# Kernel optimization log

Measured on AMD Instinct MI355X. Metric: run time of the kernel, lower is better.

## Reference

```python
import jax, jax.numpy as jnp
import numpy as np

K = 3
PAD = 1
KP = K * K


def setup_inputs() -> dict:
    key = jax.random.key(0)
    k1, k2, k3, k4 = jax.random.split(key, 4)
    B, C, O, H, W = 8, 64, 64, 128, 128
    x = jax.random.normal(k1, (B, C, H, W), dtype=jnp.float32)
    offset = jax.random.normal(k2, (B, 2 * KP, H, W), dtype=jnp.float32)
    weight = jax.random.normal(k3, (O, C, K, K), dtype=jnp.float32) * 0.05
    bias = jax.random.normal(k4, (O,), dtype=jnp.float32) * 0.05
    return {"x": x, "offset": offset, "weight": weight, "bias": bias}


def _deform_conv(x, offset, weight, bias):
    B, C, H, W = x.shape
    O = weight.shape[0]
    x_pad = jnp.pad(x, ((0, 0), (0, 0), (PAD, PAD), (PAD, PAD)))
    Hp, Wp = H + 2 * PAD, W + 2 * PAD
    dt = x.dtype

    # kernel-point grid, row-major (yy, xx) as in torch meshgrid 'ij'
    r = K // 2
    rng = jnp.arange(-r, r + 1, dtype=dt)
    ky = jnp.repeat(rng, K)          # [KP]
    kx = jnp.tile(rng, K)            # [KP]

    base_y = jnp.arange(H, dtype=dt) + PAD
    base_x = jnp.arange(W, dtype=dt) + PAD

    off = offset.reshape(B, KP, 2, H, W)
    # sample coords in padded-image space; grid_sample align_corners=True
    # normalization cancels exactly, so sample at (cy, cx) directly.
    cy = base_y[None, None, :, None] + ky[None, :, None, None] + off[:, :, 0]  # [B,KP,H,W]
    cx = base_x[None, None, None, :] + kx[None, :, None, None] + off[:, :, 1]

    y0 = jnp.floor(cy)
    x0 = jnp.floor(cx)
    wy1 = cy - y0
    wx1 = cx - x0
    wy0 = 1.0 - wy1
    wx0 = 1.0 - wx1

    flat = x_pad.reshape(B, C, Hp * Wp)

    def gather(yi, xi):
        # zeros padding: out-of-bounds corner pixels contribute 0
        valid = ((yi >= 0) & (yi <= Hp - 1) & (xi >= 0) & (xi <= Wp - 1)).astype(dt)
        yc = jnp.clip(yi, 0, Hp - 1).astype(jnp.int32)
        xc = jnp.clip(xi, 0, Wp - 1).astype(jnp.int32)
        idx = (yc * Wp + xc).reshape(B, 1, KP * H * W)
        g = jnp.take_along_axis(flat, jnp.broadcast_to(idx, (B, C, KP * H * W)), axis=2)
        g = g.reshape(B, C, KP, H, W)
        return g * valid[:, None]  # broadcast valid [B,1,KP,H,W]

    sampled = (wy0 * wx0)[:, None] * gather(y0, x0) \
            + (wy0 * wx1)[:, None] * gather(y0, x0 + 1) \
            + (wy1 * wx0)[:, None] * gather(y0 + 1, x0) \
            + (wy1 * wx1)[:, None] * gather(y0 + 1, x0 + 1)  # [B,C,KP,H,W]

    w3 = weight.reshape(O, C, KP)
    out = jnp.einsum('bcphw,ocp->bohw', sampled, w3) + bias[None, :, None, None]
    return out


def reference(x, offset, weight, bias):
    return _deform_conv(x, offset, weight, bias)
```

## Files before the change

kernel.cpp:

```cpp
#include <hip/hip_runtime.h>
#include <hip/hip_bf16.h>

#define BB 8
#define CC 64
#define OO 64
#define HH 128
#define WW 128
#define HP 130
#define WP 130
#define KP 9

typedef __attribute__((ext_vector_type(8))) short bf16x8;
typedef __attribute__((ext_vector_type(4))) float f32x4;
typedef __attribute__((ext_vector_type(4))) unsigned u32x4;

static __device__ __forceinline__ unsigned short f2bf(float f) {
  unsigned u = __float_as_uint(f);
  unsigned r = u + 0x7fffu + ((u >> 16) & 1u);
  return (unsigned short)(r >> 16);
}
static __device__ __forceinline__ f32x4 unpk4(unsigned lo, unsigned hi) {
  f32x4 r;
  r.x = __uint_as_float(lo << 16);
  r.y = __uint_as_float(lo & 0xffff0000u);
  r.z = __uint_as_float(hi << 16);
  r.w = __uint_as_float(hi & 0xffff0000u);
  return r;
}

__global__ __launch_bounds__(256) void k_xpose(const float* __restrict__ x,
                                               unsigned short* __restrict__ xt) {
  __shared__ unsigned short tile[128][66];
  int wg0 = blockIdx.x;
  int wg = (wg0 & 7) * 128 + (wg0 >> 3);
  int h = wg & 127, b = wg >> 7;
  int t = threadIdx.x;
  int w = t & 127, chalf = t >> 7;
  const float* xp = x + ((size_t)(b * CC) * HH + h) * WW;
#pragma unroll 4
  for (int c2 = 0; c2 < 32; ++c2) {
    int c = c2 * 2 + chalf;
    float v = xp[(size_t)c * HH * WW + w];
    tile[w][c] = f2bf(v);
  }
  __syncthreads();
  int c = t & 63, w2 = t >> 6;
  unsigned short* xtb = xt + (size_t)b * HP * WP * CC;
#pragma unroll 4
  for (int w4 = 0; w4 < 32; ++w4) {
    int ww = w4 * 4 + w2;
    xtb[((size_t)(h + 1) * WP + (ww + 1)) * CC + c] = tile[ww][c];
  }
  if (t < 128) {
    int xx = (t >= 64) ? (WP - 1) : 0;
    xtb[((size_t)(h + 1) * WP + xx) * CC + (t & 63)] = 0;
  }
  if (h == 0) {
    for (int i = t; i < 2 * WP * CC; i += 256) {
      int top = (i < WP * CC);
      int rem = top ? i : i - WP * CC;
      size_t y = top ? 0 : (HP - 1);
      xtb[y * WP * CC + rem] = 0;
    }
  }
}

__global__ __launch_bounds__(256) void k_wfrag(const float* __restrict__ wsrc,
                                               unsigned short* __restrict__ wf) {
  int flat = blockIdx.x * 256 + threadIdx.x;
  int j = flat & 7;
  int lane = (flat >> 3) & 63;
  int nf = (flat >> 9) & 3;
  int ks = (flat >> 11) & 1;
  int p = flat >> 12;
  int c = ks * 32 + ((lane >> 4) * 8) + j;
  int o = nf * 16 + (lane & 15);
  wf[flat] = f2bf(wsrc[(size_t)(o * CC + c) * KP + p]);
}

__global__ __launch_bounds__(256) void k_deform_main(const float* __restrict__ offset,
                                                     const float* __restrict__ bias,
                                                     const unsigned short* __restrict__ xt,
                                                     const unsigned short* __restrict__ wf,
                                                     float* __restrict__ out) {
  __shared__ __align__(16) char lds[51200];
  int wg0 = blockIdx.x;
  int wgs = (wg0 & 7) * 128 + (wg0 >> 3);
  int h = wgs & 127, b = wgs >> 7;
  int t = threadIdx.x, wave = t >> 6, lane = t & 63;

  uint4* coords = reinterpret_cast<uint4*>(lds) + wave * 288;
  char* S0 = lds + 18432;

#pragma unroll
  for (int it = 0; it < 5; ++it) {
    int pair = it * 64 + lane;
    if (pair < 288) {
      int p = pair >> 5, pxl = pair & 31;
      int w = wave * 32 + pxl;
      const float* offp = offset + (((size_t)b * 18 + 2 * p) * HH + h) * WW + w;
      float offy = offp[0];
      float offx = offp[HH * WW];
      float cy = (float)(h + p / 3) + offy;
      float cx = (float)(w + p % 3) + offx;
      float y0f = floorf(cy), x0f = floorf(cx);
      float wy1 = cy - y0f, wx1 = cx - x0f;
      int iy0 = (int)y0f, ix0 = (int)x0f;
      int iy0c = min(max(iy0, 0), HP - 1);
      int iy1c = min(max(iy0 + 1, 0), HP - 1);
      int ix0c = min(max(ix0, 0), WP - 1);
      int ix1c = min(max(ix0 + 1, 0), WP - 1);
      uint4 e;
      e.x = (unsigned)((iy0c * WP + ix0c) * (CC * 2));
      e.y = __float_as_uint(wy1);
      e.z = __float_as_uint(wx1);
      e.w = (unsigned)((ix1c - ix0c) * (CC * 2)) |
            ((unsigned)((iy1c - iy0c) * (WP * CC * 2)) << 16);
      coords[pair] = e;
    }
  }

  f32x4 acc[8];
#pragma unroll
  for (int m = 0; m < 8; ++m) acc[m] = (f32x4){0.f, 0.f, 0.f, 0.f};

  const char* xb = (const char*)(xt + (size_t)b * HP * WP * CC);
  int c8 = lane & 7, pg = lane >> 3;
  unsigned cb = (unsigned)c8 * 16;
  unsigned swz = cb ^ ((unsigned)pg << 4);
  const uint4* cwl = coords + pg;

#define GLOADX(dst, voff) \
  asm volatile("global_load_dwordx4 %0, %1, %2" \
               : "=v"(dst) : "v"(voff), "s"(xb) : "memory")
#define GLOADW(dst, voff) \
  asm volatile("global_load_dwordx4 %0, %1, %2" \
               : "=v"(dst) : "v"(voff), "s"(wf) : "memory")

  auto LOADC = [&](int p, uint4* eo) {
#pragma unroll
    for (int it = 0; it < 4; ++it) eo[it] = cwl[p * 32 + it * 8];
  };
  auto ISSUE = [&](const uint4* ei, u32x4* go) {
#pragma unroll
    for (int it = 0; it < 4; ++it) {
      unsigned dx = ei[it].w & 0xffffu, dy = ei[it].w >> 16;
      unsigned a00 = ei[it].x + cb;
      unsigned a01 = a00 + dx, a10 = a00 + dy, a11 = a10 + dx;
      GLOADX(go[it * 4 + 0], a00);
      GLOADX(go[it * 4 + 1], a01);
      GLOADX(go[it * 4 + 2], a10);
      GLOADX(go[it * 4 + 3], a11);
    }
  };
  auto BUILD = [&](const uint4* ei, const u32x4* gi, char* Sc) {
    char* swave = Sc + wave * 4096 + pg * 128;
#pragma unroll
    for (int it = 0; it < 4; ++it) {
      float wy1 = __uint_as_float(ei[it].y), wx1 = __uint_as_float(ei[it].z);
      u32x4 q00 = gi[it * 4 + 0], q01 = gi[it * 4 + 1];
      u32x4 q10 = gi[it * 4 + 2], q11 = gi[it * 4 + 3];
      f32x4 a00 = unpk4(q00.x, q00.y), a01 = unpk4(q01.x, q01.y);
      f32x4 a10 = unpk4(q10.x, q10.y), a11 = unpk4(q11.x, q11.y);
      f32x4 topA = a00 + wx1 * (a01 - a00);
      f32x4 botA = a10 + wx1 * (a11 - a10);
      f32x4 sA = topA + wy1 * (botA - topA);
      f32x4 b00 = unpk4(q00.z, q00.w), b01 = unpk4(q01.z, q01.w);
      f32x4 b10 = unpk4(q10.z, q10.w), b11 = unpk4(q11.z, q11.w);
      f32x4 topB = b00 + wx1 * (b01 - b00);
      f32x4 botB = b10 + wx1 * (b11 - b10);
      f32x4 sB = topB + wy1 * (botB - topB);
      unsigned r0, r1, r2, r3;
      asm("v_cvt_pk_bf16_f32 %0, %1, %2" : "=v"(r0) : "v"(sA.x), "v"(sA.y));
      asm("v_cvt_pk_bf16_f32 %0, %1, %2" : "=v"(r1) : "v"(sA.z), "v"(sA.w));
      asm("v_cvt_pk_bf16_f32 %0, %1, %2" : "=v"(r2) : "v"(sB.x), "v"(sB.y));
      asm("v_cvt_pk_bf16_f32 %0, %1, %2" : "=v"(r3) : "v"(sB.z), "v"(sB.w));
      u32x4 pk; pk.x = r0; pk.y = r1; pk.z = r2; pk.w = r3;
      *reinterpret_cast<u32x4*>(swave + it * 1024 + swz) = pk;
    }
  };
  auto MFMA = [&](const char* Sc, bf16x8 b0, bf16x8 b1) {
    int l15 = lane & 15, kc = (lane >> 4) * 16, sw = (lane & 7) << 4;
#pragma unroll
    for (int m = 0; m < 8; ++m) {
      int rb = (m * 16 + l15) * 128;
      bf16x8 a0 = *reinterpret_cast<const bf16x8*>(Sc + rb + (kc ^ sw));
      bf16x8 a1 = *reinterpret_cast<const bf16x8*>(Sc + rb + ((64 + kc) ^ sw));
      acc[m] = __builtin_amdgcn_mfma_f32_16x16x32_bf16(a0, b0, acc[m], 0, 0, 0);
      acc[m] = __builtin_amdgcn_mfma_f32_16x16x32_bf16(a1, b1, acc[m], 0, 0, 0);
    }
  };

  uint4 eA[4], eB[4];
  u32x4 gA[16], gB[16];
  LOADC(0, eA);
  ISSUE(eA, gA);
#pragma unroll
  for (int p = 0; p < 9; ++p) {
    char* Sc = S0 + (p & 1) * 16384;
    uint4* EC = (p & 1) ? eB : eA;
    uint4* EN = (p & 1) ? eA : eB;
    u32x4* GC = (p & 1) ? gB : gA;
    u32x4* GN = (p & 1) ? gA : gB;
    bf16x8 bv0, bv1;
    unsigned wfo0 = (unsigned)((p * 8 + wave) * 1024 + lane * 16);
    unsigned wfo1 = wfo0 + 4096;
    GLOADW(bv0, wfo0);
    GLOADW(bv1, wfo1);
    if (p < 8) LOADC(p + 1, EN);
    asm volatile("s_waitcnt vmcnt(2)" ::: "memory");
    __builtin_amdgcn_sched_barrier(0);
    BUILD(EC, GC, Sc);
    asm volatile("s_waitcnt lgkmcnt(0)" ::: "memory");
    __builtin_amdgcn_s_barrier();
    if (p < 8) {
      ISSUE(EN, GN);
      asm volatile("s_waitcnt vmcnt(16)" ::: "memory");
    } else {
      asm volatile("s_waitcnt vmcnt(0)" ::: "memory");
    }
    __builtin_amdgcn_sched_barrier(0);
    MFMA(Sc, bv0, bv1);
  }
#undef GLOADX
#undef GLOADW

  __syncthreads();
  float* S2 = reinterpret_cast<float*>(lds);
  int l15 = lane & 15;
#pragma unroll
  for (int m = 0; m < 8; ++m) {
#pragma unroll
    for (int i2 = 0; i2 < 4; ++i2) {
      int px = m * 16 + ((lane >> 4) * 4) + i2;
      int o = wave * 16 + l15;
      S2[px * 65 + o] = acc[m][i2];
    }
  }
  __syncthreads();
  {
    int px = t & 127, o2 = t >> 7;
    float* op = out + (((size_t)b * OO) * HH + h) * WW + px;
#pragma unroll
    for (int o4 = 0; o4 < 32; ++o4) {
      int o = o4 * 2 + o2;
      op[(size_t)o * HH * WW] = S2[px * 65 + o] + bias[o];
    }
  }
}

extern "C" void kernel_launch(void* const* d_in, const int* in_sizes, int n_in,
                              void* d_out, int out_size, void* d_ws, size_t ws_size,
                              hipStream_t stream) {
  const float* x = (const float*)d_in[0];
  const float* offset = (const float*)d_in[1];
  const float* weight = (const float*)d_in[2];
  const float* bias = (const float*)d_in[3];
  float* out = (float*)d_out;

  unsigned short* xt = (unsigned short*)d_ws;
  unsigned short* wf = (unsigned short*)((char*)d_ws + 17305600);

  k_xpose<<<BB * HH, 256, 0, stream>>>(x, xt);
  k_wfrag<<<144, 256, 0, stream>>>(weight, wf);
  k_deform_main<<<BB * HH, 256, 0, stream>>>(offset, bias, xt, wf, out);
}
```

Baseline: 55.76 us.

## Split each row into half-width tiles with compact coords to raise occupancy

Each workgroup now handles 64 pixels of a row instead of 128, doubling the grid and halving accumulators, gather registers and LDS (51KB to ~21KB). Per-sample coordinates are packed into 8 bytes: a base offset with two flag bits for the neighbour steps, plus the fractional weights stored as fp16. The double-buffered register sets are merged into one buffer, which is reloaded right after BUILD. The aim is more resident waves to hide gather latency, at the cost of reloading weights per tile, fp16 rounding of the interpolation weights, and less load-in-flight overlap within each wave.

```diff
diff --git a/kernel.cpp b/kernel.cpp
--- a/kernel.cpp
+++ b/kernel.cpp
@@ -13,6 +13,8 @@
 typedef __attribute__((ext_vector_type(8))) short bf16x8;
 typedef __attribute__((ext_vector_type(4))) float f32x4;
 typedef __attribute__((ext_vector_type(4))) unsigned u32x4;
+
+#define ROWB 16640u
 
 static __device__ __forceinline__ unsigned short f2bf(float f) {
   unsigned u = __float_as_uint(f);
@@ -83,21 +85,23 @@
                                                      const unsigned short* __restrict__ xt,
                                                      const unsigned short* __restrict__ wf,
                                                      float* __restrict__ out) {
-  __shared__ __align__(16) char lds[51200];
+  __shared__ __align__(16) char lds[20992];
   int wg0 = blockIdx.x;
-  int wgs = (wg0 & 7) * 128 + (wg0 >> 3);
-  int h = wgs & 127, b = wgs >> 7;
+  int wgs = (wg0 & 7) * 256 + (wg0 >> 3);
+  int tile = wgs & 1, h = (wgs >> 1) & 127, b = wgs >> 8;
+  int w0 = tile * 64;
   int t = threadIdx.x, wave = t >> 6, lane = t & 63;
 
-  uint4* coords = reinterpret_cast<uint4*>(lds) + wave * 288;
-  char* S0 = lds + 18432;
-
-#pragma unroll
-  for (int it = 0; it < 5; ++it) {
+  char* S0 = lds;
+  uint2* cw = reinterpret_cast<uint2*>(lds + 16384) + wave * 144;
+
+#pragma unroll
+  for (int it = 0; it < 3; ++it) {
     int pair = it * 64 + lane;
-    if (pair < 288) {
-      int p = pair >> 5, pxl = pair & 31;
-      int w = wave * 32 + pxl;
+    if (pair < 144) {
+      int p = pair >> 4, pxl = pair & 15;
+      int px = wave * 16 + pxl;
+      int w = w0 + px;
       const float* offp = offset + (((size_t)b * 18 + 2 * p) * HH + h) * WW + w;
       float offy = offp[0];
       float offx = offp[HH * WW];
@@ -110,25 +114,27 @@
       int iy1c = min(max(iy0 + 1, 0), HP - 1);
       int ix0c = min(max(ix0, 0), WP - 1);
       int ix1c = min(max(ix0 + 1, 0), WP - 1);
-      uint4 e;
-      e.x = (unsigned)((iy0c * WP + ix0c) * (CC * 2));
-      e.y = __float_as_uint(wy1);
-      e.z = __float_as_uint(wx1);
-      e.w = (unsigned)((ix1c - ix0c) * (CC * 2)) |
-            ((unsigned)((iy1c - iy0c) * (WP * CC * 2)) << 16);
-      coords[pair] = e;
-    }
-  }
-
-  f32x4 acc[8];
-#pragma unroll
-  for (int m = 0; m < 8; ++m) acc[m] = (f32x4){0.f, 0.f, 0.f, 0.f};
+      unsigned w0p = (unsigned)((iy0c * WP + ix0c) * (CC * 2));
+      if (ix1c != ix0c) w0p |= (1u << 30);
+      if (iy1c != iy0c) w0p |= (1u << 31);
+      unsigned hv;
+      asm("v_cvt_pkrtz_f16_f32 %0, %1, %2" : "=v"(hv) : "v"(wy1), "v"(wx1));
+      uint2 ce;
+      ce.x = w0p;
+      ce.y = hv;
+      cw[pair] = ce;
+    }
+  }
+
+  f32x4 acc[4];
+#pragma unroll
+  for (int m = 0; m < 4; ++m) acc[m] = (f32x4){0.f, 0.f, 0.f, 0.f};
 
   const char* xb = (const char*)(xt + (size_t)b * HP * WP * CC);
   int c8 = lane & 7, pg = lane >> 3;
   unsigned cb = (unsigned)c8 * 16;
   unsigned swz = cb ^ ((unsigned)pg << 4);
-  const uint4* cwl = coords + pg;
+  const uint2* cwl = cw + pg;
 
 #define GLOADX(dst, voff) \
   asm volatile("global_load_dwordx4 %0, %1, %2" \
@@ -137,15 +143,17 @@
   asm volatile("global_load_dwordx4 %0, %1, %2" \
                : "=v"(dst) : "v"(voff), "s"(wf) : "memory")
 
-  auto LOADC = [&](int p, uint4* eo) {
-#pragma unroll
-    for (int it = 0; it < 4; ++it) eo[it] = cwl[p * 32 + it * 8];
-  };
-  auto ISSUE = [&](const uint4* ei, u32x4* go) {
-#pragma unroll
-    for (int it = 0; it < 4; ++it) {
-      unsigned dx = ei[it].w & 0xffffu, dy = ei[it].w >> 16;
-      unsigned a00 = ei[it].x + cb;
+  auto LOADC = [&](int p, uint2* eo) {
+#pragma unroll
+    for (int it = 0; it < 2; ++it) eo[it] = cwl[p * 16 + it * 8];
+  };
+  auto ISSUE = [&](const uint2* ei, u32x4* go) {
+#pragma unroll
+    for (int it = 0; it < 2; ++it) {
+      unsigned w0p = ei[it].x;
+      unsigned a00 = (w0p & 0x003FFFFFu) + cb;
+      unsigned dx = ((w0p >> 30) & 1u) << 7;
+      unsigned dy = (w0p & 0x80000000u) ? ROWB : 0u;
       unsigned a01 = a00 + dx, a10 = a00 + dy, a11 = a10 + dx;
       GLOADX(go[it * 4 + 0], a00);
       GLOADX(go[it * 4 + 1], a01);
@@ -153,11 +161,14 @@
       GLOADX(go[it * 4 + 3], a11);
     }
   };
-  auto BUILD = [&](const uint4* ei, const u32x4* gi, char* Sc) {
-    char* swave = Sc + wave * 4096 + pg * 128;
-#pragma unroll
-    for (int it = 0; it < 4; ++it) {
-      float wy1 = __uint_as_float(ei[it].y), wx1 = __uint_as_float(ei[it].z);
+  auto BUILD = [&](const uint2* ei, const u32x4* gi, char* Sc) {
+    char* swave = Sc + wave * 2048 + pg * 128;
+#pragma unroll
+    for (int it = 0; it < 2; ++it) {
+      unsigned w1p = ei[it].y, w1hi = w1p >> 16;
+      float wy1, wx1;
+      asm("v_cvt_f32_f16 %0, %1" : "=v"(wy1) : "v"(w1p));
+      asm("v_cvt_f32_f16 %0, %1" : "=v"(wx1) : "v"(w1hi));
       u32x4 q00 = gi[it * 4 + 0], q01 = gi[it * 4 + 1];
       u32x4 q10 = gi[it * 4 + 2], q11 = gi[it * 4 + 3];
       f32x4 a00 = unpk4(q00.x, q00.y), a01 = unpk4(q01.x, q01.y);
@@ -182,7 +193,7 @@
   auto MFMA = [&](const char* Sc, bf16x8 b0, bf16x8 b1) {
     int l15 = lane & 15, kc = (lane >> 4) * 16, sw = (lane & 7) << 4;
 #pragma unroll
-    for (int m = 0; m < 8; ++m) {
+    for (int m = 0; m < 4; ++m) {
       int rb = (m * 16 + l15) * 128;
       bf16x8 a0 = *reinterpret_cast<const bf16x8*>(Sc + rb + (kc ^ sw));
       bf16x8 a1 = *reinterpret_cast<const bf16x8*>(Sc + rb + ((64 + kc) ^ sw));
@@ -191,31 +202,26 @@
     }
   };
 
-  uint4 eA[4], eB[4];
-  u32x4 gA[16], gB[16];
-  LOADC(0, eA);
-  ISSUE(eA, gA);
+  uint2 e[2];
+  u32x4 g[8];
+  LOADC(0, e);
+  ISSUE(e, g);
 #pragma unroll
   for (int p = 0; p < 9; ++p) {
-    char* Sc = S0 + (p & 1) * 16384;
-    uint4* EC = (p & 1) ? eB : eA;
-    uint4* EN = (p & 1) ? eA : eB;
-    u32x4* GC = (p & 1) ? gB : gA;
-    u32x4* GN = (p & 1) ? gA : gB;
+    char* Sc = S0 + (p & 1) * 8192;
     bf16x8 bv0, bv1;
-    unsigned wfo0 = (unsigned)((p * 8 + wave) * 1024 + lane * 16);
-    unsigned wfo1 = wfo0 + 4096;
-    GLOADW(bv0, wfo0);
-    GLOADW(bv1, wfo1);
-    if (p < 8) LOADC(p + 1, EN);
+    unsigned wfo = (unsigned)((p * 8 + wave) * 1024 + lane * 16);
+    GLOADW(bv0, wfo);
+    GLOADW(bv1, wfo + 4096);
     asm volatile("s_waitcnt vmcnt(2)" ::: "memory");
     __builtin_amdgcn_sched_barrier(0);
-    BUILD(EC, GC, Sc);
+    BUILD(e, g, Sc);
+    if (p < 8) LOADC(p + 1, e);
     asm volatile("s_waitcnt lgkmcnt(0)" ::: "memory");
     __builtin_amdgcn_s_barrier();
     if (p < 8) {
-      ISSUE(EN, GN);
-      asm volatile("s_waitcnt vmcnt(16)" ::: "memory");
+      ISSUE(e, g);
+      asm volatile("s_waitcnt vmcnt(8)" ::: "memory");
     } else {
       asm volatile("s_waitcnt vmcnt(0)" ::: "memory");
     }
@@ -229,7 +235,7 @@
   float* S2 = reinterpret_cast<float*>(lds);
   int l15 = lane & 15;
 #pragma unroll
-  for (int m = 0; m < 8; ++m) {
+  for (int m = 0; m < 4; ++m) {
 #pragma unroll
     for (int i2 = 0; i2 < 4; ++i2) {
       int px = m * 16 + ((lane >> 4) * 4) + i2;
@@ -239,11 +245,11 @@
   }
   __syncthreads();
   {
-    int px = t & 127, o2 = t >> 7;
-    float* op = out + (((size_t)b * OO) * HH + h) * WW + px;
-#pragma unroll
-    for (int o4 = 0; o4 < 32; ++o4) {
-      int o = o4 * 2 + o2;
+    int px = t & 63, o2 = t >> 6;
+    float* op = out + (((size_t)b * OO) * HH + h) * WW + w0 + px;
+#pragma unroll
+    for (int o4 = 0; o4 < 16; ++o4) {
+      int o = o4 * 4 + o2;
       op[(size_t)o * HH * WW] = S2[px * 65 + o] + bias[o];
     }
   }
@@ -263,5 +269,5 @@
 
   k_xpose<<<BB * HH, 256, 0, stream>>>(x, xt);
   k_wfrag<<<144, 256, 0, stream>>>(weight, wf);
-  k_deform_main<<<BB * HH, 256, 0, stream>>>(offset, bias, xt, wf, out);
-}
+  k_deform_main<<<BB * HH * 2, 256, 0, stream>>>(offset, bias, xt, wf, out);
+}
```

Measured after the change: 53.61 us. 1.04x faster.
